# Performance work log

Hardware: AMD Instinct MI355X
Metric: run time of the kernel (lower is better)

The kernel has to match this reference:

```python
import jax, jax.numpy as jnp
import numpy as np

ORDER = 7          # spline degree p
GRID = 8           # number of B-spline basis functions kept (== hidden_dim == ORDER+1)
N_KNOTS = GRID + ORDER + 1  # 16


def setup_inputs() -> dict:
    key = jax.random.key(0)
    B, S, H = 32, 4096, 8
    x = jax.random.uniform(key, (B, S, H), dtype=jnp.float32)  # in [0,1) within knot domain
    knot_vector = jnp.linspace(-1.0, 1.0, N_KNOTS, dtype=jnp.float32)  # learned param, init as in torch
    return {"x": x, "knot_vector": knot_vector}


def _bspline_basis(u, U, order, n_basis):
    """Bottom-up Cox-de Boor tabulation.
    u: [N, H] evaluation points; U: [n_knots] knot vector.
    Returns [N, H, n_basis] with N_{i,order}(u) for i in 0..n_basis-1.
    Matches the torch recursion exactly (half-open interval at degree 0,
    zero terms when a knot-difference denominator is zero)."""
    uu = u[..., None]                       # [N, H, 1]
    # degree 0: indicator U[j] <= u < U[j+1], j = 0..n_knots-2  -> [N, H, n_knots-1]
    Nb = jnp.where((U[:-1] <= uu) & (uu < U[1:]), 1.0, 0.0).astype(u.dtype)
    n_knots = U.shape[0]
    for p in range(1, order + 1):
        m = n_knots - 1 - p                 # number of degree-p splines
        Ui   = U[:m]
        Uip  = U[p:p + m]
        Ui1  = U[1:1 + m]
        Uip1 = U[p + 1:p + 1 + m]
        d1 = Uip - Ui
        d2 = Uip1 - Ui1
        w1 = jnp.where(d1 != 0, (uu - Ui) / jnp.where(d1 != 0, d1, 1.0), 0.0)
        w2 = jnp.where(d2 != 0, (Uip1 - uu) / jnp.where(d2 != 0, d2, 1.0), 0.0)
        Nb = w1 * Nb[..., :m] + w2 * Nb[..., 1:m + 1]
    return Nb[..., :n_basis]


def reference(x, knot_vector):
    B, S, H = x.shape
    u = x.reshape(B * S, H)                              # [N, H]
    basis = _bspline_basis(u, knot_vector, ORDER, GRID)  # [N, H, GRID]
    # torch: bmm(x[N,1,H], basis[N,GRID,ORDER+1]) with H==GRID==ORDER+1 ->
    # out[n,k] = sum_h u[n,h] * N_{k,ORDER}(u[n,h])
    out = jnp.einsum('nh,nhk->nk', u, basis)             # [N, H]
    return out.reshape(B, S, H)
```

## Files before the change

### kernel.cpp

```cpp
#include <hip/hip_runtime.h>


__device__ __constant__ const float kC[8][8] = {
    {    0.f,     0.f,     0.f,     0.f,    0.f,    0.f,    0.f,   1.f},
    {    1.f,     7.f,    21.f,    35.f,   35.f,   21.f,    7.f,  -7.f},
    {  120.f,   392.f,   504.f,   280.f,    0.f,  -84.f,  -42.f,  21.f},
    { 1191.f,  1715.f,   315.f,  -665.f, -315.f,  105.f,  105.f, -35.f},
    { 2416.f,     0.f, -1680.f,     0.f,  560.f,    0.f, -140.f,  35.f},
    { 1191.f, -1715.f,   315.f,   665.f, -315.f, -105.f,  105.f, -21.f},
    {  120.f,  -392.f,   504.f,  -280.f,    0.f,   84.f,  -42.f,   7.f},
    {    1.f,    -7.f,    21.f,   -35.f,   35.f,  -21.f,    7.f,  -1.f},
};

__global__ __launch_bounds__(256) void bspline_kernel(
    const float* __restrict__ x,
    const float* __restrict__ knots,
    float* __restrict__ out,
    int npts)
{
    int t0 = blockIdx.x * blockDim.x + threadIdx.x;
    if (t0 >= npts) return;

    const float u = x[t0];

    const float U0 = knots[0], U15 = knots[15];
    const float s = (u - U0) * (15.0f / (U15 - U0));

    const float fl = floorf(s);
    const float t  = s - fl;
    const int   ji = (int)fl;
    const int   sg = ji - 7;

    float pv[8];
#pragma unroll
    for (int m = 0; m < 8; ++m) {
        float p = kC[m][7];
#pragma unroll
        for (int d = 6; d >= 0; --d) p = fmaf(p, t, kC[m][d]);
        pv[m] = p;
    }

    float Q[8];
#pragma unroll
    for (int i = 0; i < 8; ++i) Q[i] = pv[7 - i];

    const bool b4 = (sg & 4) != 0;
    const bool b2 = (sg & 2) != 0;
    const bool b1 = (sg & 1) != 0;
#pragma unroll
    for (int k = 7; k >= 0; --k) Q[k] = b4 ? (k >= 4 ? Q[k - 4] : 0.0f) : Q[k];
#pragma unroll
    for (int k = 7; k >= 0; --k) Q[k] = b2 ? (k >= 2 ? Q[k - 2] : 0.0f) : Q[k];
#pragma unroll
    for (int k = 7; k >= 0; --k) Q[k] = b1 ? (k >= 1 ? Q[k - 1] : 0.0f) : Q[k];

    const float up = u * (1.0f / 5040.0f);
    float v[8];
#pragma unroll
    for (int k = 0; k < 8; ++k) v[k] = up * Q[k];

    const int h = threadIdx.x & 7;
    const bool c2 = (h & 4) != 0, c1 = (h & 2) != 0, c0 = (h & 1) != 0;

    float a4[4];
#pragma unroll
    for (int r = 0; r < 4; ++r) {
        float send = c2 ? v[r] : v[r + 4];
        float keep = c2 ? v[r + 4] : v[r];
        a4[r] = keep + __shfl_xor(send, 4);
    }
    float a2[2];
#pragma unroll
    for (int r = 0; r < 2; ++r) {
        float send = c1 ? a4[r] : a4[r + 2];
        float keep = c1 ? a4[r + 2] : a4[r];
        a2[r] = keep + __shfl_xor(send, 2);
    }
    {
        float send = c0 ? a2[0] : a2[1];
        float keep = c0 ? a2[1] : a2[0];
        out[t0] = keep + __shfl_xor(send, 1);
    }
}

extern "C" void kernel_launch(void* const* d_in, const int* in_sizes, int n_in,
                              void* d_out, int out_size, void* d_ws, size_t ws_size,
                              hipStream_t stream) {
    const float* x     = (const float*)d_in[0];
    const float* knots = (const float*)d_in[1];
    float* out         = (float*)d_out;

    const int npts = in_sizes[0];
    const int block = 256;
    const int grid  = (npts + block - 1) / block;
    bspline_kernel<<<grid, block, 0, stream>>>(x, knots, out, npts);
}
```

Baseline: 10.12 us.

## Process two points per thread with even/odd split polynomial evaluation

Each thread now loads a float2 (two adjacent points), evaluates the basis for both, sums the per-channel contributions locally, and needs one fewer shuffle stage in the reduction, writing a float2. The eight degree-7 polynomials are rewritten around t-0.5 as symmetric even/odd parts, so each pair of mirrored polynomials shares one evaluation in q^2. This cuts FMA count, shuffle count and thread count, at the cost of more registers per thread and assuming the point count is even.

```diff
diff --git a/kernel.cpp b/kernel.cpp
--- a/kernel.cpp
+++ b/kernel.cpp
@@ -1,43 +1,37 @@
 #include <hip/hip_runtime.h>
 
 
-__device__ __constant__ const float kC[8][8] = {
-    {    0.f,     0.f,     0.f,     0.f,    0.f,    0.f,    0.f,   1.f},
-    {    1.f,     7.f,    21.f,    35.f,   35.f,   21.f,    7.f,  -7.f},
-    {  120.f,   392.f,   504.f,   280.f,    0.f,  -84.f,  -42.f,  21.f},
-    { 1191.f,  1715.f,   315.f,  -665.f, -315.f,  105.f,  105.f, -35.f},
-    { 2416.f,     0.f, -1680.f,     0.f,  560.f,    0.f, -140.f,  35.f},
-    { 1191.f, -1715.f,   315.f,   665.f, -315.f, -105.f,  105.f, -21.f},
-    {  120.f,  -392.f,   504.f,  -280.f,    0.f,   84.f,  -42.f,   7.f},
-    {    1.f,    -7.f,    21.f,   -35.f,   35.f,  -21.f,    7.f,  -1.f},
-};
-
-__global__ __launch_bounds__(256) void bspline_kernel(
-    const float* __restrict__ x,
-    const float* __restrict__ knots,
-    float* __restrict__ out,
-    int npts)
+static __device__ __forceinline__ void eval_point(
+    float u, float U0, float sc, float v[8])
 {
-    int t0 = blockIdx.x * blockDim.x + threadIdx.x;
-    if (t0 >= npts) return;
-
-    const float u = x[t0];
-
-    const float U0 = knots[0], U15 = knots[15];
-    const float s = (u - U0) * (15.0f / (U15 - U0));
-
+    const float s  = (u - U0) * sc;
     const float fl = floorf(s);
     const float t  = s - fl;
-    const int   ji = (int)fl;
-    const int   sg = ji - 7;
+    const int   sg = (int)fl - 7;
+
+    const float q  = t - 0.5f;
+    const float q2 = q * q;
+
+    constexpr float kS[4][4] = {
+        {   0.0078125f,    0.65625f,    4.375f,   3.5f},
+        {  17.0234375f,  154.21875f,   83.125f, -17.5f},
+        { 473.8828125f,  793.40625f, -275.625f,  31.5f},
+        {2029.0859375f, -948.28125f,  188.125f, -17.5f},
+    };
+    constexpr float kD[4][4] = {
+        {   0.109375f,      2.1875f,     5.25f,   1.0f},
+        {  78.859375f,    159.6875f,     5.25f,  -7.0f},
+        {1074.171875f,     10.9375f,   -99.75f,  21.0f},
+        {1422.421875f,   -846.5625f,   236.25f, -35.0f},
+    };
 
     float pv[8];
 #pragma unroll
-    for (int m = 0; m < 8; ++m) {
-        float p = kC[m][7];
-#pragma unroll
-        for (int d = 6; d >= 0; --d) p = fmaf(p, t, kC[m][d]);
-        pv[m] = p;
+    for (int m = 0; m < 4; ++m) {
+        float S = fmaf(fmaf(fmaf(kS[m][3], q2, kS[m][2]), q2, kS[m][1]), q2, kS[m][0]);
+        float D = fmaf(fmaf(fmaf(kD[m][3], q2, kD[m][2]), q2, kD[m][1]), q2, kD[m][0]);
+        pv[m]     = fmaf( q, D, S);
+        pv[7 - m] = fmaf(-q, D, S);
     }
 
     float Q[8];
@@ -55,32 +49,52 @@
     for (int k = 7; k >= 0; --k) Q[k] = b1 ? (k >= 1 ? Q[k - 1] : 0.0f) : Q[k];
 
     const float up = u * (1.0f / 5040.0f);
-    float v[8];
 #pragma unroll
     for (int k = 0; k < 8; ++k) v[k] = up * Q[k];
+}
 
-    const int h = threadIdx.x & 7;
-    const bool c2 = (h & 4) != 0, c1 = (h & 2) != 0, c0 = (h & 1) != 0;
+__global__ __launch_bounds__(256) void bspline_kernel(
+    const float* __restrict__ x,
+    const float* __restrict__ knots,
+    float* __restrict__ out,
+    int npairs)
+{
+    const int tid = blockIdx.x * blockDim.x + threadIdx.x;
+    if (tid >= npairs) return;
 
-    float a4[4];
+    const float U0 = knots[0], U15 = knots[15];
+    const float sc = 15.0f / (U15 - U0);
+
+    const float2 uu = reinterpret_cast<const float2*>(x)[tid];
+
+    float v0[8], v1[8];
+    eval_point(uu.x, U0, sc, v0);
+    eval_point(uu.y, U0, sc, v1);
+
+    float w[8];
+#pragma unroll
+    for (int k = 0; k < 8; ++k) w[k] = v0[k] + v1[k];
+
+    const int a = threadIdx.x & 3;
+    const bool hb2 = (a & 2) != 0;
+    const bool hb1 = (a & 1) != 0;
+
+    float s4[4];
 #pragma unroll
     for (int r = 0; r < 4; ++r) {
-        float send = c2 ? v[r] : v[r + 4];
-        float keep = c2 ? v[r + 4] : v[r];
-        a4[r] = keep + __shfl_xor(send, 4);
+        float send = hb2 ? w[r] : w[r + 4];
+        float keep = hb2 ? w[r + 4] : w[r];
+        s4[r] = keep + __shfl_xor(send, 2);
     }
-    float a2[2];
+    float s2[2];
 #pragma unroll
     for (int r = 0; r < 2; ++r) {
-        float send = c1 ? a4[r] : a4[r + 2];
-        float keep = c1 ? a4[r + 2] : a4[r];
-        a2[r] = keep + __shfl_xor(send, 2);
+        float send = hb1 ? s4[r] : s4[r + 2];
+        float keep = hb1 ? s4[r + 2] : s4[r];
+        s2[r] = keep + __shfl_xor(send, 1);
     }
-    {
-        float send = c0 ? a2[0] : a2[1];
-        float keep = c0 ? a2[1] : a2[0];
-        out[t0] = keep + __shfl_xor(send, 1);
-    }
+
+    reinterpret_cast<float2*>(out)[tid] = make_float2(s2[0], s2[1]);
 }
 
 extern "C" void kernel_launch(void* const* d_in, const int* in_sizes, int n_in,
@@ -90,8 +104,10 @@
     const float* knots = (const float*)d_in[1];
     float* out         = (float*)d_out;
 
-    const int npts = in_sizes[0];
+    const int npts   = in_sizes[0];
+    const int npairs = npts / 2;
+
     const int block = 256;
-    const int grid  = (npts + block - 1) / block;
-    bspline_kernel<<<grid, block, 0, stream>>>(x, knots, out, npts);
+    const int grid  = (npairs + block - 1) / block;
+    bspline_kernel<<<grid, block, 0, stream>>>(x, knots, out, npairs);
 }
```

After: 9.737 us. -3.8%, faster.
